# Kernel optimization log

Measured on AMD Instinct MI355X. Metric: run time of the kernel, lower is better.

## Reference

```python
import jax, jax.numpy as jnp
import numpy as np

NUM_EXPERTS = 8
HIDDEN = 2048
INTER = 4096
TOKENS = 8192
TOP_K = 2


def relu2(x):
    # Nemotron-H 'relu2': squared ReLU
    r = jax.nn.relu(x)
    return r * r


def setup_inputs() -> dict:
    key = jax.random.key(0)
    k1, k2, k3, k4, k5 = jax.random.split(key, 5)
    hidden_states = jax.random.normal(k1, (TOKENS, HIDDEN), dtype=jnp.float32)
    top_k_index = jax.random.randint(k2, (TOKENS, TOP_K), 0, NUM_EXPERTS, dtype=jnp.int64)
    top_k_weights = jax.random.uniform(k3, (TOKENS, TOP_K), dtype=jnp.float32)
    up_proj = jax.random.normal(k4, (NUM_EXPERTS, INTER, HIDDEN), dtype=jnp.float32) * 0.02
    down_proj = jax.random.normal(k5, (NUM_EXPERTS, HIDDEN, INTER), dtype=jnp.float32) * 0.02
    return {
        "hidden_states": hidden_states,
        "top_k_index": top_k_index,
        "top_k_weights": top_k_weights,
        "up_proj": up_proj,
        "down_proj": down_proj,
    }


def reference(hidden_states, top_k_index, top_k_weights, up_proj, down_proj):
    num_experts = up_proj.shape[0]
    # combine weight per (token, expert): sum over top-k slots routed to that expert
    # (equivalent to the one-hot mask + per-slot top_k_weights in the torch loop)
    onehot = (top_k_index[:, :, None] == jnp.arange(num_experts)[None, None, :])  # [T, K, E]
    combine = jnp.sum(onehot * top_k_weights[:, :, None], axis=1)  # [T, E]
    out = jnp.zeros_like(hidden_states)
    # fixed small loop over experts (structural, not a data dim)
    for e in range(num_experts):
        h = relu2(hidden_states @ up_proj[e].T)  # [T, I]
        y = h @ down_proj[e].T  # [T, H]
        out = out + combine[:, e:e + 1] * y
    return out
```

## Files before the change

kernel.cpp:

```cpp
#include <hip/hip_runtime.h>

#define T_TOKENS 8192
#define H_DIM    2048
#define I_DIM    4096
#define NE       8
#define NPAIR    16384
#define PADBM    256
#define PADP     (NPAIR + NE * PADBM)
#define RT_MAX   (PADP / PADBM)

#define BM2 256
#define BN2 256
#define BK2 64
#define NTHR 512
#define NKT_UP (H_DIM / BK2)
#define NKT_DN (I_DIM / BK2)
#define NTN_UP (I_DIM / BN2)
#define NTN_DN (H_DIM / BN2)
#define TILE_B 32768
#define TILE_S 16384

#define WS_AB   0ull
#define WS_W    (WS_AB + (size_t)RT_MAX * NKT_UP * TILE_B)
#define WS_H    (WS_W + (size_t)NE * I_DIM * H_DIM * 2)
#define WS_TOK  (WS_H + (size_t)RT_MAX * NKT_DN * TILE_B)
#define WS_META (WS_TOK + (size_t)PADP * 4)

typedef __attribute__((ext_vector_type(8))) short bf16x8;
typedef __attribute__((ext_vector_type(4))) float f32x4;

__device__ __forceinline__ unsigned short f2bf(float f) {
  union { float f; unsigned u; } a; a.f = f;
  unsigned r = a.u + 0x7fffu + ((a.u >> 16) & 1u);
  return (unsigned short)(r >> 16);
}

__device__ __forceinline__ float b2f(unsigned short b) {
  union { unsigned u; float f; } a; a.u = ((unsigned)b) << 16;
  return a.f;
}

__device__ __forceinline__ bf16x8 pack8(float4 a, float4 b) {
  bf16x8 o;
  o[0] = (short)f2bf(a.x); o[1] = (short)f2bf(a.y);
  o[2] = (short)f2bf(a.z); o[3] = (short)f2bf(a.w);
  o[4] = (short)f2bf(b.x); o[5] = (short)f2bf(b.y);
  o[6] = (short)f2bf(b.z); o[7] = (short)f2bf(b.w);
  return o;
}

__device__ __forceinline__ void gload16(const void* g, void* l) {
  __builtin_amdgcn_global_load_lds(
      (const __attribute__((address_space(1))) unsigned int*)g,
      (__attribute__((address_space(3))) unsigned int*)l,
      16, 0, 0);
}

__device__ __forceinline__ int swz(int a) { return a ^ ((a >> 2) & 0x60); }

__global__ __launch_bounds__(512) void route_all(const int* __restrict__ idx,
                                                 int* __restrict__ meta,
                                                 int* __restrict__ tok) {
  __shared__ int cnt[NE], base[NE + 1], cur[NE];
  int t = threadIdx.x;
  if (t < NE) { cnt[t] = 0; cur[t] = 0; }
  for (int i = t; i < PADP; i += 512) tok[i] = -1;
  __syncthreads();
  for (int i = t; i < NPAIR; i += 512) atomicAdd(&cnt[idx[i]], 1);
  __syncthreads();
  if (t == 0) {
    int off = 0;
    for (int e = 0; e < NE; ++e) {
      base[e] = off;
      off += ((cnt[e] + PADBM - 1) / PADBM) * PADBM;
    }
    base[NE] = off;
    for (int e = 0; e <= NE; ++e) meta[16 + e] = base[e];
  }
  __syncthreads();
  for (int i = t; i < NPAIR; i += 512) {
    int e = idx[i];
    int pos = base[e] + atomicAdd(&cur[e], 1);
    tok[pos] = i;
  }
}

__global__ __launch_bounds__(512) void cvt_tile_w(
    const float* __restrict__ W, unsigned short* __restrict__ out,
    int NKT, int K) {
  __shared__ float4 ltq[TILE_B / 16];
  char* lt = (char*)ltq;
  int kt = blockIdx.x % NKT, panel = blockIdx.x / NKT;
  int t = threadIdx.x, r = t >> 1, half = t & 1;
  const float* src = W + ((size_t)panel * 256 + r) * K + kt * 64 + half * 32;
  float4 v[8];
  #pragma unroll
  for (int i = 0; i < 8; ++i) v[i] = ((const float4*)src)[i];
  #pragma unroll
  for (int i2 = 0; i2 < 4; ++i2) {
    int c = half * 4 + i2;
    *(bf16x8*)(lt + swz(c * 4096 + r * 16)) = pack8(v[2 * i2], v[2 * i2 + 1]);
  }
  __syncthreads();
  char* dst = (char*)(out + (size_t)blockIdx.x * TILE_S);
  int tb = t * 16;
  #pragma unroll
  for (int i = 0; i < 4; ++i) {
    int o = i * 8192 + tb;
    *(bf16x8*)(dst + o) = *(const bf16x8*)(lt + swz(o));
  }
}

__global__ __launch_bounds__(512) void gather_tile_x(
    const float* __restrict__ x, const int* __restrict__ tok,
    unsigned short* __restrict__ out) {
  __shared__ float4 ltq[TILE_B / 16];
  char* lt = (char*)ltq;
  int kt = blockIdx.x & (NKT_UP - 1), rt = blockIdx.x >> 5;
  int t = threadIdx.x, r = t >> 1, half = t & 1;
  int v = tok[rt * 256 + r];
  bf16x8 pk[4];
  if (v < 0) {
    #pragma unroll
    for (int i2 = 0; i2 < 4; ++i2) pk[i2] = (bf16x8)0;
  } else {
    const float* src = x + (size_t)(v >> 1) * H_DIM + kt * 64 + half * 32;
    float4 w[8];
    #pragma unroll
    for (int i = 0; i < 8; ++i) w[i] = ((const float4*)src)[i];
    #pragma unroll
    for (int i2 = 0; i2 < 4; ++i2) pk[i2] = pack8(w[2 * i2], w[2 * i2 + 1]);
  }
  #pragma unroll
  for (int i2 = 0; i2 < 4; ++i2) {
    int c = half * 4 + i2;
    *(bf16x8*)(lt + swz(c * 4096 + r * 16)) = pk[i2];
  }
  __syncthreads();
  char* dst = (char*)(out + (size_t)blockIdx.x * TILE_S);
  int tb = t * 16;
  #pragma unroll
  for (int i = 0; i < 4; ++i) {
    int o = i * 8192 + tb;
    *(bf16x8*)(dst + o) = *(const bf16x8*)(lt + swz(o));
  }
}


#define STAGE_FULL(KT, BS) do {                                                \
    const char* aT_ = aTile + (size_t)(KT) * TILE_B;                           \
    const char* bT_ = bTile + (size_t)(KT) * TILE_B;                           \
    _Pragma("unroll")                                                          \
    for (int l_ = 0; l_ < 4; ++l_) {                                           \
      int off_ = (l_ * 8 + wv) * 1024 + lane16;                                \
      gload16(aT_ + off_, smem + (BS) * 32768 + off_);                         \
      gload16(bT_ + off_, smem + 65536 + (BS) * 32768 + off_);                 \
    }                                                                          \
  } while (0)

#define STAGE_Q(KT, BS, Q) do {                                                \
    const char* aT_ = aTile + (size_t)(KT) * TILE_B;                           \
    const char* bT_ = bTile + (size_t)(KT) * TILE_B;                           \
    int off_ = ((Q) * 8 + wv) * 1024 + lane16;                                 \
    gload16(aT_ + off_, smem + (BS) * 32768 + off_);                           \
    gload16(bT_ + off_, smem + 65536 + (BS) * 32768 + off_);                   \
  } while (0)

#define PHASE(KS, FH, DO_STAGE, DO_VM) do {                                    \
    bf16x8 af[4];                                                              \
    const char* aB_ = smem + bufc * 32768 + ((KS) * 4 + hi) * 4096;            \
    _Pragma("unroll")                                                          \
    for (int f = 0; f < 4; ++f)                                                \
      af[f] = *(const bf16x8*)(aB_ + arow_b + ((FH) * 4 + f) * 256);           \
    if ((FH) == 0) {                                                           \
      const char* bB_ = smem + 65536 + bufc * 32768 + ((KS) * 4 + hi) * 4096;  \
      _Pragma("unroll")                                                        \
      for (int f = 0; f < 4; ++f)                                              \
        bfr[f] = *(const bf16x8*)(bB_ + brow_b + f * 256);                     \
    }                                                                          \
    DO_STAGE;                                                                  \
    DO_VM;                                                                     \
    __builtin_amdgcn_s_barrier();                                              \
    asm volatile("s_waitcnt lgkmcnt(0)" ::: "memory");                         \
    __builtin_amdgcn_s_setprio(1);                                             \
    _Pragma("unroll")                                                          \
    for (int fm = 0; fm < 4; ++fm)                                             \
      _Pragma("unroll")                                                        \
      for (int fn = 0; fn < 4; ++fn)                                           \
        acc[(FH) * 4 + fm][fn] = __builtin_amdgcn_mfma_f32_16x16x32_bf16(      \
            af[fm], bfr[fn], acc[(FH) * 4 + fm][fn], 0, 0, 0);                 \
    __builtin_amdgcn_s_setprio(0);                                             \
    __builtin_amdgcn_s_barrier();                                              \
  } while (0)

#define GEMM_PROLOGUE()                                                        \
  STAGE_FULL(0, 0);                                                            \
  asm volatile("s_waitcnt vmcnt(4)" ::: "memory");                             \
  __builtin_amdgcn_s_barrier();

#define GEMM_MAIN(NKT)                                                         \
  int bufc = 0;                                                                \
  for (int kt = 0; kt < (NKT); ++kt) {                                         \
    int ktn = (kt + 1 < (NKT)) ? kt + 1 : (NKT) - 1;  \
    int bn_ = bufc ^ 1;                                                        \
    PHASE(0, 0, STAGE_Q(ktn, bn_, 0), (void)0);                                \
    PHASE(0, 1, STAGE_Q(ktn, bn_, 1),                                          \
          asm volatile("s_waitcnt vmcnt(4)" ::: "memory"));                    \
    PHASE(1, 0, STAGE_Q(ktn, bn_, 2), (void)0);                                \
    PHASE(1, 1, STAGE_Q(ktn, bn_, 3),                                          \
          asm volatile("s_waitcnt vmcnt(4)" ::: "memory"));                    \
    bufc ^= 1;                                                                 \
  }

__device__ __forceinline__ void rt_nt_decode(int bid, int NTN, int& rt, int& nt) {
  int xcd = bid & 7, g = bid >> 3;
  int gh = NTN >> 1;
  int gn = g % gh, gr = g / gh;
  rt = gr * 4 + (xcd >> 1);
  nt = gn * 2 + (xcd & 1);
}

__global__ __launch_bounds__(NTHR, 2) void gemm_up8(
    const unsigned short* __restrict__ Ab, const unsigned short* __restrict__ Wt,
    unsigned short* __restrict__ Hb, const int* __restrict__ meta) {
  extern __shared__ char smem[];
  const int* pstart = meta + 16;
  int rt, nt;
  rt_nt_decode(blockIdx.x, NTN_UP, rt, nt);
  int row0 = rt * BM2;
  if (row0 >= pstart[NE]) return;
  int e = 0;
  #pragma unroll
  for (int q = 1; q < NE; ++q) if (row0 >= pstart[q]) e = q;

  int tid = threadIdx.x;
  int wv = tid >> 6, lane = tid & 63;
  int lane16 = lane * 16;

  const char* aTile = (const char*)Ab + (size_t)rt * NKT_UP * TILE_B;
  const char* bTile = (const char*)Wt + (size_t)(e * NTN_UP + nt) * NKT_UP * TILE_B;

  int wm = wv >> 2, wn = wv & 3;
  int hi = lane >> 4;
  int arow_b = (wm * 128 + (lane & 15)) * 16;
  int brow_b = (wn * 64 + (lane & 15)) * 16;

  f32x4 acc[8][4] = {};
  bf16x8 bfr[4];

  GEMM_PROLOGUE();
  GEMM_MAIN(NKT_UP);

  unsigned short* baseT = Hb + ((size_t)rt * NKT_DN + nt * 4 + wn) * TILE_S
                             + ((lane & 15) >> 3) * 2048 + (lane & 7);
  #pragma unroll
  for (int fm = 0; fm < 8; ++fm) {
    #pragma unroll
    for (int j = 0; j < 4; ++j) {
      int r = wm * 128 + hi * 4 + fm * 16 + j;
      unsigned short* rb = baseT + r * 8;
      #pragma unroll
      for (int fn = 0; fn < 4; ++fn) {
        float v = acc[fm][fn][j];
        v = v > 0.f ? v * v : 0.f;
        rb[fn * 4096] = f2bf(v);
      }
    }
  }
}

__global__ __launch_bounds__(NTHR, 2) void gemm_down8(
    const unsigned short* __restrict__ Hb, const unsigned short* __restrict__ Wt,
    unsigned short* __restrict__ Yb, const int* __restrict__ meta,
    const int* __restrict__ tok) {
  extern __shared__ char smem[];
  const int* pstart = meta + 16;
  int rt, nt;
  rt_nt_decode(blockIdx.x, NTN_DN, rt, nt);
  int row0 = rt * BM2;
  if (row0 >= pstart[NE]) return;
  int e = 0;
  #pragma unroll
  for (int q = 1; q < NE; ++q) if (row0 >= pstart[q]) e = q;

  int tid = threadIdx.x;
  int wv = tid >> 6, lane = tid & 63;
  int lane16 = lane * 16;

  const char* aTile = (const char*)Hb + (size_t)rt * NKT_DN * TILE_B;
  const char* bTile = (const char*)Wt + (size_t)(e * NTN_DN + nt) * NKT_DN * TILE_B;

  int wm = wv >> 2, wn = wv & 3;
  int hi = lane >> 4;
  int arow_b = (wm * 128 + (lane & 15)) * 16;
  int brow_b = (wn * 64 + (lane & 15)) * 16;

  f32x4 acc[8][4] = {};
  bf16x8 bfr[4];

  GEMM_PROLOGUE();
  GEMM_MAIN(NKT_DN);

  int crow0 = row0 + wm * 128 + hi * 4;
  int ccol0 = nt * BN2 + wn * 64 + (lane & 15);
  #pragma unroll
  for (int fm = 0; fm < 8; ++fm) {
    #pragma unroll
    for (int j = 0; j < 4; ++j) {
      int p = crow0 + fm * 16 + j;
      int i = tok[p];
      if (i < 0) continue;
      unsigned short* dst = Yb + (size_t)i * H_DIM + ccol0;
      #pragma unroll
      for (int fn = 0; fn < 4; ++fn)
        dst[fn * 16] = f2bf(acc[fm][fn][j]);
    }
  }
}

__global__ __launch_bounds__(256) void combine(
    const unsigned short* __restrict__ Yb, const float* __restrict__ tkw,
    float* __restrict__ out) {
  int h0 = threadIdx.x * 8;
  #pragma unroll
  for (int tt = 0; tt < 4; ++tt) {
    int t = blockIdx.x * 4 + tt;
    float w0 = tkw[2 * t], w1 = tkw[2 * t + 1];
    bf16x8 ya = *(const bf16x8*)(Yb + (size_t)(2 * t) * H_DIM + h0);
    bf16x8 yb = *(const bf16x8*)(Yb + (size_t)(2 * t + 1) * H_DIM + h0);
    float* dst = out + (size_t)t * H_DIM + h0;
    float4 o0, o1;
    o0.x = w0 * b2f((unsigned short)ya[0]) + w1 * b2f((unsigned short)yb[0]);
    o0.y = w0 * b2f((unsigned short)ya[1]) + w1 * b2f((unsigned short)yb[1]);
    o0.z = w0 * b2f((unsigned short)ya[2]) + w1 * b2f((unsigned short)yb[2]);
    o0.w = w0 * b2f((unsigned short)ya[3]) + w1 * b2f((unsigned short)yb[3]);
    o1.x = w0 * b2f((unsigned short)ya[4]) + w1 * b2f((unsigned short)yb[4]);
    o1.y = w0 * b2f((unsigned short)ya[5]) + w1 * b2f((unsigned short)yb[5]);
    o1.z = w0 * b2f((unsigned short)ya[6]) + w1 * b2f((unsigned short)yb[6]);
    o1.w = w0 * b2f((unsigned short)ya[7]) + w1 * b2f((unsigned short)yb[7]);
    ((float4*)dst)[0] = o0;
    ((float4*)dst)[1] = o1;
  }
}

extern "C" void kernel_launch(void* const* d_in, const int* in_sizes, int n_in,
                              void* d_out, int out_size, void* d_ws, size_t ws_size,
                              hipStream_t stream) {
  const float* x   = (const float*)d_in[0];
  const int*   tki = (const int*)d_in[1];
  const float* tkw = (const float*)d_in[2];
  const float* up  = (const float*)d_in[3];
  const float* dn  = (const float*)d_in[4];
  float* out = (float*)d_out;
  char* ws = (char*)d_ws;

  unsigned short* ab  = (unsigned short*)(ws + WS_AB);
  unsigned short* wt  = (unsigned short*)(ws + WS_W);
  unsigned short* hb  = (unsigned short*)(ws + WS_H);
  int*            tok = (int*)(ws + WS_TOK);
  unsigned short* yb  = (unsigned short*)(ws + WS_AB);
  int*            meta= (int*)(ws + WS_META);

  hipFuncSetAttribute((const void*)gemm_up8,
                      hipFuncAttributeMaxDynamicSharedMemorySize, 131072);
  hipFuncSetAttribute((const void*)gemm_down8,
                      hipFuncAttributeMaxDynamicSharedMemorySize, 131072);

  route_all<<<1, 512, 0, stream>>>(tki, meta, tok);

  gather_tile_x<<<RT_MAX * NKT_UP, 512, 0, stream>>>(x, tok, ab);
  cvt_tile_w<<<NE * NTN_UP * NKT_UP, 512, 0, stream>>>(up, wt, NKT_UP, H_DIM);

  gemm_up8<<<RT_MAX * NTN_UP, NTHR, 131072, stream>>>(ab, wt, hb, meta);

  cvt_tile_w<<<NE * NTN_DN * NKT_DN, 512, 0, stream>>>(dn, wt, NKT_DN, I_DIM);

  gemm_down8<<<RT_MAX * NTN_DN, NTHR, 131072, stream>>>(hb, wt, yb, meta, tok);

  combine<<<T_TOKENS / 4, 256, 0, stream>>>(yb, tkw, out);
}
```

Before: 862.3 us.

## Fuse down-proj weight conversion into up-GEMM launch as extra blocks

Appends the down-projection weight conversion tiles as extra thread blocks of the up-projection GEMM kernel, writing into a separate workspace buffer so it cannot clobber the up weights still being read. The aim is to overlap the memory-bound conversion with the tail of the compute-bound GEMM and to drop one kernel launch. If the workspace is too small, it falls back to the old sequential path. Costs are extra workspace, plus conversion blocks that may compete with GEMM blocks for CUs and shared memory, since they launch with 128KB of dynamic LDS.

```diff
diff --git a/kernel.cpp b/kernel.cpp
--- a/kernel.cpp
+++ b/kernel.cpp
@@ -20,11 +20,13 @@
 #define TILE_B 32768
 #define TILE_S 16384
 
-#define WS_AB   0ull
-#define WS_W    (WS_AB + (size_t)RT_MAX * NKT_UP * TILE_B)
-#define WS_H    (WS_W + (size_t)NE * I_DIM * H_DIM * 2)
-#define WS_TOK  (WS_H + (size_t)RT_MAX * NKT_DN * TILE_B)
-#define WS_META (WS_TOK + (size_t)PADP * 4)
+#define G_UP   (RT_MAX * NTN_UP)
+#define G_CVTD (NE * NTN_DN * NKT_DN)
+
+#define AB_BYTES  ((size_t)RT_MAX * NKT_UP * TILE_B)
+#define W_BYTES   ((size_t)NE * I_DIM * H_DIM * 2)
+#define HB_BYTES  ((size_t)RT_MAX * NKT_DN * TILE_B)
+#define TOK_BYTES ((size_t)PADP * 4)
 
 typedef __attribute__((ext_vector_type(8))) short bf16x8;
 typedef __attribute__((ext_vector_type(4))) float f32x4;
@@ -85,30 +87,35 @@
   }
 }
 
+__device__ __forceinline__ void cvt_tile_body(
+    const float* __restrict__ W, unsigned short* __restrict__ out,
+    int tile, int NKT, int K, char* lt) {
+  int kt = tile % NKT, panel = tile / NKT;
+  int t = threadIdx.x, r = t >> 1, half = t & 1;
+  const float* src = W + ((size_t)panel * 256 + r) * K + kt * 64 + half * 32;
+  float4 v[8];
+  #pragma unroll
+  for (int i = 0; i < 8; ++i) v[i] = ((const float4*)src)[i];
+  #pragma unroll
+  for (int i2 = 0; i2 < 4; ++i2) {
+    int c = half * 4 + i2;
+    *(bf16x8*)(lt + swz(c * 4096 + r * 16)) = pack8(v[2 * i2], v[2 * i2 + 1]);
+  }
+  __syncthreads();
+  char* dst = (char*)(out + (size_t)tile * TILE_S);
+  int tb = t * 16;
+  #pragma unroll
+  for (int i = 0; i < 4; ++i) {
+    int o = i * 8192 + tb;
+    *(bf16x8*)(dst + o) = *(const bf16x8*)(lt + swz(o));
+  }
+}
+
 __global__ __launch_bounds__(512) void cvt_tile_w(
     const float* __restrict__ W, unsigned short* __restrict__ out,
     int NKT, int K) {
   __shared__ float4 ltq[TILE_B / 16];
-  char* lt = (char*)ltq;
-  int kt = blockIdx.x % NKT, panel = blockIdx.x / NKT;
-  int t = threadIdx.x, r = t >> 1, half = t & 1;
-  const float* src = W + ((size_t)panel * 256 + r) * K + kt * 64 + half * 32;
-  float4 v[8];
-  #pragma unroll
-  for (int i = 0; i < 8; ++i) v[i] = ((const float4*)src)[i];
-  #pragma unroll
-  for (int i2 = 0; i2 < 4; ++i2) {
-    int c = half * 4 + i2;
-    *(bf16x8*)(lt + swz(c * 4096 + r * 16)) = pack8(v[2 * i2], v[2 * i2 + 1]);
-  }
-  __syncthreads();
-  char* dst = (char*)(out + (size_t)blockIdx.x * TILE_S);
-  int tb = t * 16;
-  #pragma unroll
-  for (int i = 0; i < 4; ++i) {
-    int o = i * 8192 + tb;
-    *(bf16x8*)(dst + o) = *(const bf16x8*)(lt + swz(o));
-  }
+  cvt_tile_body(W, out, blockIdx.x, NKT, K, (char*)ltq);
 }
 
 __global__ __launch_bounds__(512) void gather_tile_x(
@@ -220,10 +227,16 @@
   nt = gn * 2 + (xcd & 1);
 }
 
-__global__ __launch_bounds__(NTHR, 2) void gemm_up8(
-    const unsigned short* __restrict__ Ab, const unsigned short* __restrict__ Wt,
-    unsigned short* __restrict__ Hb, const int* __restrict__ meta) {
+__global__ __launch_bounds__(NTHR, 2) void gemm_up8f(
+    const unsigned short* __restrict__ Ab, const unsigned short* __restrict__ WtU,
+    unsigned short* __restrict__ Hb, const int* __restrict__ meta,
+    const float* __restrict__ dnW, unsigned short* __restrict__ WtD,
+    int nGemm) {
   extern __shared__ char smem[];
+  if ((int)blockIdx.x >= nGemm) {
+    cvt_tile_body(dnW, WtD, (int)blockIdx.x - nGemm, NKT_DN, I_DIM, smem);
+    return;
+  }
   const int* pstart = meta + 16;
   int rt, nt;
   rt_nt_decode(blockIdx.x, NTN_UP, rt, nt);
@@ -238,7 +251,7 @@
   int lane16 = lane * 16;
 
   const char* aTile = (const char*)Ab + (size_t)rt * NKT_UP * TILE_B;
-  const char* bTile = (const char*)Wt + (size_t)(e * NTN_UP + nt) * NKT_UP * TILE_B;
+  const char* bTile = (const char*)WtU + (size_t)(e * NTN_UP + nt) * NKT_UP * TILE_B;
 
   int wm = wv >> 2, wn = wv & 3;
   int hi = lane >> 4;
@@ -354,14 +367,19 @@
   float* out = (float*)d_out;
   char* ws = (char*)d_ws;
 
-  unsigned short* ab  = (unsigned short*)(ws + WS_AB);
-  unsigned short* wt  = (unsigned short*)(ws + WS_W);
-  unsigned short* hb  = (unsigned short*)(ws + WS_H);
-  int*            tok = (int*)(ws + WS_TOK);
-  unsigned short* yb  = (unsigned short*)(ws + WS_AB);
-  int*            meta= (int*)(ws + WS_META);
-
-  hipFuncSetAttribute((const void*)gemm_up8,
+  size_t need_fused = AB_BYTES + 2 * W_BYTES + HB_BYTES + TOK_BYTES + 128;
+  bool fused = ws_size >= need_fused;
+
+  unsigned short* ab  = (unsigned short*)ws;
+  unsigned short* wtU = (unsigned short*)(ws + AB_BYTES);
+  unsigned short* wtD = fused ? (unsigned short*)(ws + AB_BYTES + W_BYTES) : wtU;
+  char* pHB = (char*)wtD + W_BYTES;
+  unsigned short* hb  = (unsigned short*)pHB;
+  int*            tok = (int*)(pHB + HB_BYTES);
+  int*            meta= (int*)(pHB + HB_BYTES + TOK_BYTES);
+  unsigned short* yb  = ab;
+
+  hipFuncSetAttribute((const void*)gemm_up8f,
                       hipFuncAttributeMaxDynamicSharedMemorySize, 131072);
   hipFuncSetAttribute((const void*)gemm_down8,
                       hipFuncAttributeMaxDynamicSharedMemorySize, 131072);
@@ -369,13 +387,17 @@
   route_all<<<1, 512, 0, stream>>>(tki, meta, tok);
 
   gather_tile_x<<<RT_MAX * NKT_UP, 512, 0, stream>>>(x, tok, ab);
-  cvt_tile_w<<<NE * NTN_UP * NKT_UP, 512, 0, stream>>>(up, wt, NKT_UP, H_DIM);
-
-  gemm_up8<<<RT_MAX * NTN_UP, NTHR, 131072, stream>>>(ab, wt, hb, meta);
-
-  cvt_tile_w<<<NE * NTN_DN * NKT_DN, 512, 0, stream>>>(dn, wt, NKT_DN, I_DIM);
-
-  gemm_down8<<<RT_MAX * NTN_DN, NTHR, 131072, stream>>>(hb, wt, yb, meta, tok);
+  cvt_tile_w<<<NE * NTN_UP * NKT_UP, 512, 0, stream>>>(up, wtU, NKT_UP, H_DIM);
+
+  if (fused) {
+    gemm_up8f<<<G_UP + G_CVTD, NTHR, 131072, stream>>>(ab, wtU, hb, meta,
+                                                       dn, wtD, G_UP);
+  } else {
+    gemm_up8f<<<G_UP, NTHR, 131072, stream>>>(ab, wtU, hb, meta, dn, wtD, G_UP);
+    cvt_tile_w<<<G_CVTD, 512, 0, stream>>>(dn, wtD, NKT_DN, I_DIM);
+  }
+
+  gemm_down8<<<RT_MAX * NTN_DN, NTHR, 131072, stream>>>(hb, wtD, yb, meta, tok);
 
   combine<<<T_TOKENS / 4, 256, 0, stream>>>(yb, tkw, out);
 }
```

Result: faster. 823.9 us (-4.5%).
